# Kernel optimization log

Hardware: AMD Instinct MI355X
Metric: run time of the kernel (lower is better)

Reference implementation:

```python
import jax, jax.numpy as jnp
import numpy as np

N = 100000
E = 1600000
IN_DIM = 128
OUT_DIM = 128
NEG_SLOPE = 0.01  # F.leaky_relu default


def setup_inputs() -> dict:
    key = jax.random.key(0)
    k1, k2, k3, k4, k5, k6 = jax.random.split(key, 6)
    feat = jax.random.normal(k1, (N, IN_DIM), dtype=jnp.float32)
    biclique_mask = jax.random.uniform(k2, (IN_DIM,), dtype=jnp.float32)
    W = jax.random.normal(k3, (OUT_DIM, IN_DIM), dtype=jnp.float32) * 0.05
    attn = jax.random.normal(k4, (OUT_DIM,), dtype=jnp.float32) * 0.1
    src = jax.random.randint(k5, (E,), 0, N, dtype=jnp.int32)
    dst = jax.random.randint(k6, (E,), 0, N, dtype=jnp.int32)
    return {"feat": feat, "biclique_mask": biclique_mask, "W": W,
            "attn": attn, "src": src, "dst": dst}


def reference(feat, biclique_mask, W, attn, src, dst):
    # h = Linear(feat * mask), no bias
    h = (feat * biclique_mask[None, :]) @ W.T            # [N, out_dim]
    # edge score depends only on src node -> compute per-node then gather
    s = jax.nn.leaky_relu(h @ attn, negative_slope=NEG_SLOPE)  # [N]
    score = s[src]                                        # [E]
    # edge softmax grouped by destination node
    seg_max = jax.ops.segment_max(score, dst, num_segments=N)  # [N]
    seg_max = jnp.where(jnp.isfinite(seg_max), seg_max, 0.0)   # empty segs
    ex = jnp.exp(score - seg_max[dst])                     # [E]
    denom = jax.ops.segment_sum(ex, dst, num_segments=N)   # [N]
    a = ex / denom[dst]                                    # [E]
    # weighted aggregation: sum_{e: dst(e)=v} h[src(e)] * a[e]
    m = h[src] * a[:, None]                                # [E, out_dim]
    h_new = jax.ops.segment_sum(m, dst, num_segments=N)    # [N, out_dim]
    return jax.nn.relu(h_new)
```

## Files before the change

### kernel.cpp

```cpp
#include <hip/hip_runtime.h>
#include <math.h>

#define NN 100000
#define EE 1600000
#define DIM 128

#define BK 512
#define NBK2 196
#define NCH 256
#define EPB 6250
#define SCN (NBK2 * NCH)
#define NSB 49

typedef _Float16 half8 __attribute__((ext_vector_type(8)));
typedef _Float16 half2v __attribute__((ext_vector_type(2)));
typedef float f32x4 __attribute__((ext_vector_type(4)));

__global__ __launch_bounds__(256) void k_wt(const float* __restrict__ W,
                                            const float* __restrict__ mask,
                                            _Float16* __restrict__ Bt) {
    int o = blockIdx.x * 256 + threadIdx.x;
    if (o < DIM * DIM) Bt[o] = (_Float16)(W[o] * mask[o & 127]);
}

__global__ __launch_bounds__(256) void k_gemm(const float* __restrict__ feat,
                                              const _Float16* __restrict__ Bt,
                                              const float* __restrict__ attn,
                                              _Float16* __restrict__ hh,
                                              float* __restrict__ s) {
    const int lane = threadIdx.x & 63;
    const int wv   = threadIdx.x >> 6;
    const int l15  = lane & 15;
    const int quad = lane >> 4;
    const int row0 = blockIdx.x * 64 + wv * 16;

    f32x4 acc[8];
#pragma unroll
    for (int nt = 0; nt < 8; ++nt) acc[nt] = (f32x4){0.f, 0.f, 0.f, 0.f};

    const int arow = row0 + l15;
    const bool okA = arow < NN;
    const float* ap = feat + (size_t)(okA ? arow : 0) * DIM + quad * 8;

#pragma unroll
    for (int kc = 0; kc < 4; ++kc) {
        half8 a;
        float4 f0 = ((const float4*)(ap + kc * 32))[0];
        float4 f1 = ((const float4*)(ap + kc * 32))[1];
        if (!okA) { f0 = make_float4(0, 0, 0, 0); f1 = make_float4(0, 0, 0, 0); }
        a[0] = (_Float16)f0.x; a[1] = (_Float16)f0.y;
        a[2] = (_Float16)f0.z; a[3] = (_Float16)f0.w;
        a[4] = (_Float16)f1.x; a[5] = (_Float16)f1.y;
        a[6] = (_Float16)f1.z; a[7] = (_Float16)f1.w;
#pragma unroll
        for (int nt = 0; nt < 8; ++nt) {
            half8 b = *(const half8*)(Bt + (size_t)(nt * 16 + l15) * DIM + kc * 32 + quad * 8);
            acc[nt] = __builtin_amdgcn_mfma_f32_16x16x32_f16(a, b, acc[nt], 0, 0, 0);
        }
    }

    float avv[8];
#pragma unroll
    for (int nt = 0; nt < 8; ++nt) avv[nt] = attn[nt * 16 + l15];

#pragma unroll
    for (int r = 0; r < 4; ++r) {
        int row = row0 + quad * 4 + r;
        float p = 0.f;
#pragma unroll
        for (int nt = 0; nt < 8; ++nt) p += acc[nt][r] * avv[nt];
        p += __shfl_xor(p, 1, 64);
        p += __shfl_xor(p, 2, 64);
        p += __shfl_xor(p, 4, 64);
        p += __shfl_xor(p, 8, 64);
        if (l15 == 0 && row < NN) {
            float lr = (p > 0.f) ? p : 0.01f * p;
            s[row] = __expf(lr);
        }
    }

#pragma unroll
    for (int nt = 0; nt < 8; ++nt) {
#pragma unroll
        for (int r = 0; r < 4; ++r) {
            int row = row0 + quad * 4 + r;
            if (row < NN)
                hh[(size_t)row * DIM + nt * 16 + l15] = (_Float16)acc[nt][r];
        }
    }
}

__global__ __launch_bounds__(1024) void k_bhist(const int* __restrict__ dst,
                                                int* __restrict__ gHist) {
    __shared__ int hist[NBK2];
    const int t = threadIdx.x, b = blockIdx.x;
    for (int i = t; i < NBK2; i += 1024) hist[i] = 0;
    __syncthreads();
    const int e0 = b * EPB;
    int e1 = e0 + EPB; if (e1 > EE) e1 = EE;
    for (int e = e0 + t; e < e1; e += 1024)
        atomicAdd(&hist[dst[e] >> 9], 1);
    __syncthreads();
    for (int i = t; i < NBK2; i += 1024)
        gHist[i * NCH + b] = hist[i];
}

__global__ __launch_bounds__(256) void k_scan_a(const int* __restrict__ deg,
                                                int* __restrict__ excl,
                                                int* __restrict__ bsum) {
    __shared__ int wsum[4];
    __shared__ int woff[4];
    const int t = threadIdx.x, b = blockIdx.x;
    const int base = b * 1024 + t * 4;
    int v0 = deg[base + 0];
    int v1 = deg[base + 1];
    int v2 = deg[base + 2];
    int v3 = deg[base + 3];
    int tsum = v0 + v1 + v2 + v3;

    const int lane = t & 63, w = t >> 6;
    int incl = tsum;
#pragma unroll
    for (int d = 1; d < 64; d <<= 1) {
        int n = __shfl_up(incl, d, 64);
        if (lane >= d) incl += n;
    }
    if (lane == 63) wsum[w] = incl;
    __syncthreads();
    if (t == 0) {
        int run = 0;
#pragma unroll
        for (int i = 0; i < 4; ++i) { woff[i] = run; run += wsum[i]; }
        bsum[b] = run;
    }
    __syncthreads();
    int texcl = incl - tsum + woff[w];
    excl[base + 0] = texcl;
    excl[base + 1] = texcl + v0;
    excl[base + 2] = texcl + v0 + v1;
    excl[base + 3] = texcl + v0 + v1 + v2;
}

__global__ __launch_bounds__(64) void k_scan_b(const int* __restrict__ bsum,
                                               int* __restrict__ boff) {
    const int lane = threadIdx.x & 63;
    int v = (lane < NSB) ? bsum[lane] : 0;
    int incl = v;
#pragma unroll
    for (int d = 1; d < 64; d <<= 1) {
        int n = __shfl_up(incl, d, 64);
        if (lane >= d) incl += n;
    }
    if (lane < NSB) boff[lane] = incl - v;
}

__global__ __launch_bounds__(1024) void k_bscatter(const int* __restrict__ src,
                                                   const int* __restrict__ dst,
                                                   const float* __restrict__ s,
                                                   const int* __restrict__ gOff,
                                                   const int* __restrict__ boff,
                                                   int2* __restrict__ binned) {
    __shared__ int cur[NBK2];
    const int t = threadIdx.x, b = blockIdx.x;
    for (int i = t; i < NBK2; i += 1024) {
        int idx = i * NCH + b;
        cur[i] = gOff[idx] + boff[idx >> 10];
    }
    __syncthreads();
    const int e0 = b * EPB;
    int e1 = e0 + EPB; if (e1 > EE) e1 = EE;
    for (int e = e0 + t; e < e1; e += 1024) {
        int d  = dst[e];
        int si = src[e];
        float x = s[si];
        int bk   = d >> 9;
        int dloc = d & (BK - 1);
        int pos = atomicAdd(&cur[bk], 1);
        binned[pos] = make_int2(si | (dloc << 20), __float_as_int(x));
    }
}

__global__ __launch_bounds__(1024) void k_group(const int* __restrict__ gOff,
                                                const int* __restrict__ boff,
                                                const int2* __restrict__ binned,
                                                int2* __restrict__ pack,
                                                int* __restrict__ offs) {
    __shared__ int ldeg[BK];
    __shared__ int wpart[8];
    const int bk = blockIdx.x;
    const int t  = threadIdx.x;
    const int i0 = bk * NCH;
    const int base = gOff[i0] + boff[i0 >> 10];
    int endp;
    if (bk == NBK2 - 1) endp = EE;
    else {
        int i1 = (bk + 1) * NCH;
        endp = gOff[i1] + boff[i1 >> 10];
    }

    if (t < BK) ldeg[t] = 0;
    __syncthreads();
    for (int j = base + t; j < endp; j += 1024)
        atomicAdd(&ldeg[(binned[j].x >> 20) & (BK - 1)], 1);
    __syncthreads();

    int v = 0, incl = 0;
    const int lane = t & 63;
    if (t < BK) {
        v = ldeg[t];
        incl = v;
#pragma unroll
        for (int d = 1; d < 64; d <<= 1) {
            int n = __shfl_up(incl, d, 64);
            if (lane >= d) incl += n;
        }
        if (lane == 63) wpart[t >> 6] = incl;
    }
    __syncthreads();
    if (t == 0) {
        int run = 0;
#pragma unroll
        for (int i = 0; i < 8; ++i) { int tmp = wpart[i]; wpart[i] = run; run += tmp; }
    }
    __syncthreads();
    if (t < BK) {
        int excl = incl - v + wpart[t >> 6];
        int c = base + excl;
        int n = bk * BK + t;
        if (n < NN) offs[n] = c;
        ldeg[t] = c;
    }
    if (bk == NBK2 - 1 && t == 0) offs[NN] = EE;
    __syncthreads();

    for (int j = base + t; j < endp; j += 1024) {
        int2 e = binned[j];
        int dloc = (e.x >> 20) & (BK - 1);
        int si   = e.x & 0xFFFFF;
        int pos = atomicAdd(&ldeg[dloc], 1);
        pack[pos] = make_int2(si, e.y);
    }
}

__global__ __launch_bounds__(256) void k_agg(const _Float16* __restrict__ hh,
                                             const int* __restrict__ offs,
                                             const int2* __restrict__ pack,
                                             float* __restrict__ out) {
    const int lane = threadIdx.x & 63;
    const int wid  = __builtin_amdgcn_readfirstlane(blockIdx.x * 4 + (threadIdx.x >> 6));
    if (wid >= NN) return;
    const int beg = __builtin_amdgcn_readfirstlane(offs[wid]);
    const int end = __builtin_amdgcn_readfirstlane(offs[wid + 1]);

    const half2v* h2 = (const half2v*)hh;
    float l = 0.f;
    float2 acc[4];
#pragma unroll
    for (int j = 0; j < 4; ++j) acc[j] = make_float2(0.f, 0.f);

    int p = beg;
    for (; p + 8 <= end; p += 8) {
        int2 e[8];
#pragma unroll
        for (int j = 0; j < 8; ++j) e[j] = pack[p + j];
        half2v v[8];
#pragma unroll
        for (int j = 0; j < 8; ++j) v[j] = h2[((unsigned)e[j].x << 6) + lane];
#pragma unroll
        for (int j = 0; j < 8; ++j) {
            float w = __int_as_float(e[j].y);
            acc[j & 3].x = fmaf((float)v[j][0], w, acc[j & 3].x);
            acc[j & 3].y = fmaf((float)v[j][1], w, acc[j & 3].y);
            l += w;
        }
    }
    const int rem = end - p;
    if (rem > 0) {
        const int last = end - 1;
        int2 e[7];
#pragma unroll
        for (int j = 0; j < 7; ++j) {
            int q = p + j;
            e[j] = pack[q <= last ? q : last];
        }
        half2v v[7];
#pragma unroll
        for (int j = 0; j < 7; ++j) v[j] = h2[((unsigned)e[j].x << 6) + lane];
#pragma unroll
        for (int j = 0; j < 7; ++j) {
            float w = (j < rem) ? __int_as_float(e[j].y) : 0.f;
            acc[j & 3].x = fmaf((float)v[j][0], w, acc[j & 3].x);
            acc[j & 3].y = fmaf((float)v[j][1], w, acc[j & 3].y);
            l += w;
        }
    }

    float inv = (l > 0.f) ? (1.0f / l) : 0.f;
    float rx = fmaxf((acc[0].x + acc[1].x + acc[2].x + acc[3].x) * inv, 0.f);
    float ry = fmaxf((acc[0].y + acc[1].y + acc[2].y + acc[3].y) * inv, 0.f);
    ((float2*)out)[(size_t)wid * 64 + lane] = make_float2(rx, ry);
}

extern "C" void kernel_launch(void* const* d_in, const int* in_sizes, int n_in,
                              void* d_out, int out_size, void* d_ws, size_t ws_size,
                              hipStream_t stream) {
    const float* feat = (const float*)d_in[0];
    const float* mask = (const float*)d_in[1];
    const float* W    = (const float*)d_in[2];
    const float* attn = (const float*)d_in[3];
    const int*   src  = (const int*)d_in[4];
    const int*   dst  = (const int*)d_in[5];
    float* out = (float*)d_out;

    char* ws = (char*)d_ws;
    size_t off = 0;
    auto alloc = [&](size_t bytes) -> void* {
        void* p = ws + off;
        off = (off + bytes + 511) & ~(size_t)511;
        return p;
    };
    _Float16* hh  = (_Float16*)alloc((size_t)NN * DIM * 2);
    float*  sv    = (float*)alloc((size_t)NN * 4);
    _Float16* Bt  = (_Float16*)alloc((size_t)DIM * DIM * 2);
    int*    gOff  = (int*)alloc((size_t)SCN * 4);
    int*    offs  = (int*)alloc((size_t)(NN + 1) * 4);
    int*    bsum  = (int*)alloc((size_t)NSB * 4);
    int*    boff  = (int*)alloc((size_t)NSB * 4);
    int2*   binned= (int2*)alloc((size_t)EE * 8);
    int2*   pack  = (int2*)alloc((size_t)EE * 8);

    k_wt<<<(DIM * DIM + 255) / 256, 256, 0, stream>>>(W, mask, Bt);
    k_gemm<<<(NN + 63) / 64, 256, 0, stream>>>(feat, Bt, attn, hh, sv);
    k_bhist<<<NCH, 1024, 0, stream>>>(dst, gOff);
    k_scan_a<<<NSB, 256, 0, stream>>>(gOff, gOff, bsum);
    k_scan_b<<<1, 64, 0, stream>>>(bsum, boff);
    k_bscatter<<<NCH, 1024, 0, stream>>>(src, dst, sv, gOff, boff, binned);
    k_group<<<NBK2, 1024, 0, stream>>>(gOff, boff, binned, pack, offs);
    k_agg<<<(NN + 3) / 4, 256, 0, stream>>>(hh, offs, pack, out);
}
```

Baseline: 244.0 us.

## Split each wavefront into four edge groups with 16-byte feature gathers

The aggregation kernel now splits each 64-lane wavefront into four groups of 16 lanes. Each group handles a different edge and gathers a full 256-byte fp16 row with 16-byte half8 loads, instead of every lane gathering a 4-byte half2 for one edge at a time. Partial sums are reduced across groups with cross-lane shuffles, and one group writes the output with float4 stores. This cuts the number of memory instructions and widens each gather. In exchange it adds shuffle reductions, leaves lanes idle at the store, and issues fewer independent loads per iteration (two per lane instead of eight), which may reduce memory-level parallelism.

```diff
diff --git a/kernel.cpp b/kernel.cpp
--- a/kernel.cpp
+++ b/kernel.cpp
@@ -247,58 +247,79 @@
                                              const int2* __restrict__ pack,
                                              float* __restrict__ out) {
     const int lane = threadIdx.x & 63;
+    const int g    = lane >> 4;
+    const int li   = lane & 15;
     const int wid  = __builtin_amdgcn_readfirstlane(blockIdx.x * 4 + (threadIdx.x >> 6));
     if (wid >= NN) return;
     const int beg = __builtin_amdgcn_readfirstlane(offs[wid]);
     const int end = __builtin_amdgcn_readfirstlane(offs[wid + 1]);
 
-    const half2v* h2 = (const half2v*)hh;
+    const half8* h8 = (const half8*)hh;
+    float acc[8];
+#pragma unroll
+    for (int k = 0; k < 8; ++k) acc[k] = 0.f;
     float l = 0.f;
-    float2 acc[4];
-#pragma unroll
-    for (int j = 0; j < 4; ++j) acc[j] = make_float2(0.f, 0.f);
 
     int p = beg;
     for (; p + 8 <= end; p += 8) {
-        int2 e[8];
-#pragma unroll
-        for (int j = 0; j < 8; ++j) e[j] = pack[p + j];
-        half2v v[8];
-#pragma unroll
-        for (int j = 0; j < 8; ++j) v[j] = h2[((unsigned)e[j].x << 6) + lane];
-#pragma unroll
-        for (int j = 0; j < 8; ++j) {
-            float w = __int_as_float(e[j].y);
-            acc[j & 3].x = fmaf((float)v[j][0], w, acc[j & 3].x);
-            acc[j & 3].y = fmaf((float)v[j][1], w, acc[j & 3].y);
-            l += w;
-        }
-    }
+        int2 e0 = pack[p + g];
+        int2 e1 = pack[p + 4 + g];
+        half8 v0 = h8[((unsigned)e0.x << 4) + li];
+        half8 v1 = h8[((unsigned)e1.x << 4) + li];
+        float w0 = __int_as_float(e0.y);
+        float w1 = __int_as_float(e1.y);
+#pragma unroll
+        for (int k = 0; k < 8; ++k) acc[k] = fmaf((float)v0[k], w0, acc[k]);
+#pragma unroll
+        for (int k = 0; k < 8; ++k) acc[k] = fmaf((float)v1[k], w1, acc[k]);
+        l += w0 + w1;
+    }
+
     const int rem = end - p;
     if (rem > 0) {
         const int last = end - 1;
-        int2 e[7];
-#pragma unroll
-        for (int j = 0; j < 7; ++j) {
-            int q = p + j;
-            e[j] = pack[q <= last ? q : last];
-        }
-        half2v v[7];
-#pragma unroll
-        for (int j = 0; j < 7; ++j) v[j] = h2[((unsigned)e[j].x << 6) + lane];
-#pragma unroll
-        for (int j = 0; j < 7; ++j) {
-            float w = (j < rem) ? __int_as_float(e[j].y) : 0.f;
-            acc[j & 3].x = fmaf((float)v[j][0], w, acc[j & 3].x);
-            acc[j & 3].y = fmaf((float)v[j][1], w, acc[j & 3].y);
-            l += w;
-        }
-    }
+        int q0 = p + g;
+        int2 e0 = pack[q0 <= last ? q0 : last];
+        half8 v0 = h8[((unsigned)e0.x << 4) + li];
+        float w0 = (g < rem) ? __int_as_float(e0.y) : 0.f;
+#pragma unroll
+        for (int k = 0; k < 8; ++k) acc[k] = fmaf((float)v0[k], w0, acc[k]);
+        l += w0;
+        if (rem > 4) {
+            int q1 = p + 4 + g;
+            int2 e1 = pack[q1 <= last ? q1 : last];
+            half8 v1 = h8[((unsigned)e1.x << 4) + li];
+            float w1 = (4 + g < rem) ? __int_as_float(e1.y) : 0.f;
+#pragma unroll
+            for (int k = 0; k < 8; ++k) acc[k] = fmaf((float)v1[k], w1, acc[k]);
+            l += w1;
+        }
+    }
+
+#pragma unroll
+    for (int k = 0; k < 8; ++k) {
+        acc[k] += __shfl_xor(acc[k], 16, 64);
+        acc[k] += __shfl_xor(acc[k], 32, 64);
+    }
+    l += __shfl_xor(l, 16, 64);
+    l += __shfl_xor(l, 32, 64);
 
     float inv = (l > 0.f) ? (1.0f / l) : 0.f;
-    float rx = fmaxf((acc[0].x + acc[1].x + acc[2].x + acc[3].x) * inv, 0.f);
-    float ry = fmaxf((acc[0].y + acc[1].y + acc[2].y + acc[3].y) * inv, 0.f);
-    ((float2*)out)[(size_t)wid * 64 + lane] = make_float2(rx, ry);
+
+    if (g == 0) {
+        float4 o0, o1;
+        o0.x = fmaxf(acc[0] * inv, 0.f);
+        o0.y = fmaxf(acc[1] * inv, 0.f);
+        o0.z = fmaxf(acc[2] * inv, 0.f);
+        o0.w = fmaxf(acc[3] * inv, 0.f);
+        o1.x = fmaxf(acc[4] * inv, 0.f);
+        o1.y = fmaxf(acc[5] * inv, 0.f);
+        o1.z = fmaxf(acc[6] * inv, 0.f);
+        o1.w = fmaxf(acc[7] * inv, 0.f);
+        float4* op = (float4*)(out + (size_t)wid * DIM + li * 8);
+        op[0] = o0;
+        op[1] = o1;
+    }
 }
 
 extern "C" void kernel_launch(void* const* d_in, const int* in_sizes, int n_in,
```

Measured after the change: 246.0 us. Within noise of the previous version (+0.8%).
